# Kernel optimization log

Hardware: AMD Instinct MI355X
Metric: run time of the kernel (lower is better)

The kernel has to match this reference:

```python
import jax, jax.numpy as jnp
import numpy as np
import math

B, L, D, H = 4, 2048, 1024, 16
DK = D // H


def setup_inputs() -> dict:
    key = jax.random.key(0)
    ks = jax.random.split(key, 12)
    scale = math.sqrt(6.0 / (D + D))  # xavier_uniform for square Linear
    def lin(k):
        return jax.random.uniform(k, (D, D), jnp.float32, -scale, scale)
    inp = {
        "query": jax.random.normal(ks[0], (B, L, D), jnp.float32),
        "key": jax.random.normal(ks[1], (B, L, D), jnp.float32),
        "value": jax.random.normal(ks[2], (B, L, D), jnp.float32),
        "Wq": lin(ks[3]), "bq": jnp.zeros((D,), jnp.float32),
        "Wk": lin(ks[4]), "bk": jnp.zeros((D,), jnp.float32),
        "Wv": lin(ks[5]), "bv": jnp.zeros((D,), jnp.float32),
        "Wo": lin(ks[6]), "bo": jnp.zeros((D,), jnp.float32),
        # causal mask: True means masked (hide future positions)
        "attn_mask": jnp.triu(jnp.ones((L, L), dtype=bool), k=1),
    }
    return inp


def reference(query, key, value, Wq, bq, Wk, bk, Wv, bv, Wo, bo, attn_mask):
    def proj(x, W, b):
        # torch Linear: x @ W.T + b ; then split heads -> [B, H, L, DK]
        y = jnp.einsum('bld,ed->ble', x, W) + b
        return y.reshape(B, L, H, DK).transpose(0, 2, 1, 3)

    q = proj(query, Wq, bq)
    k = proj(key, Wk, bk)
    v = proj(value, Wv, bv)

    scores = jnp.einsum('bhqd,bhkd->bhqk', q, k) / jnp.sqrt(jnp.float32(DK))
    scores = jnp.where(attn_mask[None, None, :, :], jnp.float32(-jnp.inf), scores)
    p_attn = jax.nn.softmax(scores, axis=-1)  # dropout p=0 (eval)

    ctx = jnp.einsum('bhqk,bhkd->bhqd', p_attn, v)
    ctx = ctx.transpose(0, 2, 1, 3).reshape(B, L, D)
    out = jnp.einsum('bld,ed->ble', ctx, Wo) + bo
    return out
```

## Files before the change

kernel.cpp:

```cpp
#include <hip/hip_runtime.h>
#include <hip/hip_bf16.h>
#include <stdint.h>

typedef unsigned short u16;
typedef unsigned int u32;
typedef short short8 __attribute__((ext_vector_type(8)));
typedef float f32x4 __attribute__((ext_vector_type(4)));
typedef u32 u32x4 __attribute__((ext_vector_type(4)));
typedef u32 u32x2 __attribute__((ext_vector_type(2)));

#define DEV static __device__ __forceinline__

constexpr int Bsz = 4, Lseq = 2048, Dm = 1024, Hn = 16, Dk = 64;
constexpr float LOG2E = 1.44269504088896340736f;
constexpr float QSCALE = 0.125f * LOG2E;

DEV u16 f2bf(float x) {
    u32 u = __builtin_bit_cast(u32, x);
    return (u16)((u + 0x7fffu + ((u >> 16) & 1u)) >> 16);
}

DEV u32 pk2(float a, float b) {
    __hip_bfloat162 h = __float22bfloat162_rn(float2{a, b});
    u32 r;
    __builtin_memcpy(&r, &h, 4);
    return r;
}

DEV u32x4 ld8_cvt(const float* p) {
    f32x4 lo = *(const f32x4*)p;
    f32x4 hi = *(const f32x4*)(p + 4);
    u32x4 r;
    r[0] = pk2(lo[0], lo[1]);
    r[1] = pk2(lo[2], lo[3]);
    r[2] = pk2(hi[0], hi[1]);
    r[3] = pk2(hi[2], hi[3]);
    return r;
}

DEV void glds16(const void* g, void* l) {
    __builtin_amdgcn_global_load_lds(
        (const __attribute__((address_space(1))) void*)g,
        (__attribute__((address_space(3))) void*)l, 16, 0, 0);
}

__global__ __launch_bounds__(256) void cvt_f2b(
    const float* __restrict__ s, u16* __restrict__ d, int n8)
{
    int i = blockIdx.x * 256 + threadIdx.x;
    if (i >= n8) return;
    ((u32x4*)d)[i] = ld8_cvt(s + (long)i * 8);
}

template <int MODE>
__global__ __launch_bounds__(256) void gemm_glds(
    const u16* __restrict__ A, const u16* __restrict__ Bw,
    const float* __restrict__ bias, void* __restrict__ Cout, float scale)
{
    __shared__ u16 At[2][128 * 32];
    __shared__ u16 Bt[2][128 * 32];

    const int tid = threadIdx.x;
    const int lane = tid & 63, wid = tid >> 6;
    const int wr = wid >> 1, wc = wid & 1;
    const int mbase = blockIdx.x * 128, nbase = blockIdx.y * 128;

    f32x4 acc[4][4];
#pragma unroll
    for (int i = 0; i < 4; i++)
#pragma unroll
        for (int j = 0; j < 4; j++) acc[i][j] = (f32x4)0.f;

    const int srow = lane >> 2;
    const int sseg = (lane & 3) * 8;

    auto stage = [&](int kt, int buf) {
#pragma unroll
        for (int c = 0; c < 2; c++) {
            const int sec = wid * 2 + c;
            const long ko = (long)kt * 32 + sseg;
            glds16(A + (long)(mbase + sec * 16 + srow) * Dm + ko, &At[buf][sec * 512]);
            glds16(Bw + (long)(nbase + sec * 16 + srow) * Dm + ko, &Bt[buf][sec * 512]);
        }
    };

    stage(0, 0);
    __syncthreads();

    for (int kt = 0; kt < 32; kt++) {
        const int cur = kt & 1;
        if (kt + 1 < 32) stage(kt + 1, cur ^ 1);
        short8 af[4], bfr[4];
#pragma unroll
        for (int mf = 0; mf < 4; mf++)
            af[mf] = *(const short8*)&At[cur][(wr * 64 + mf * 16 + (lane & 15)) * 32 + (lane >> 4) * 8];
#pragma unroll
        for (int nf = 0; nf < 4; nf++)
            bfr[nf] = *(const short8*)&Bt[cur][(wc * 64 + nf * 16 + (lane & 15)) * 32 + (lane >> 4) * 8];
        __builtin_amdgcn_s_setprio(1);
#pragma unroll
        for (int mf = 0; mf < 4; mf++)
#pragma unroll
            for (int nf = 0; nf < 4; nf++)
                acc[mf][nf] = __builtin_amdgcn_mfma_f32_16x16x32_bf16(af[mf], bfr[nf], acc[mf][nf], 0, 0, 0);
        __builtin_amdgcn_s_setprio(0);
        __syncthreads();
    }

#pragma unroll
    for (int nf = 0; nf < 4; nf++) {
        const int n = nbase + wc * 64 + nf * 16 + (lane & 15);
        const float bv = bias[n];
#pragma unroll
        for (int mf = 0; mf < 4; mf++) {
            const int m0 = mbase + wr * 64 + mf * 16 + (lane >> 4) * 4;
#pragma unroll
            for (int r = 0; r < 4; r++) {
                const int m = m0 + r;
                const float v = (acc[mf][nf][r] + bv) * scale;
                if (MODE == 0) {
                    int b = m >> 11, l = m & 2047, h = n >> 6, dk = n & 63;
                    long addr = ((long)(b * Hn + h) * Lseq + l) * Dk + dk;
                    ((u16*)Cout)[addr] = f2bf(v);
                } else {
                    ((float*)Cout)[(long)m * Dm + n] = v;
                }
            }
        }
    }
}

template <int MODE, int A32>
__global__ __launch_bounds__(256) void gemm_bt(
    const void* __restrict__ Xv, const float* __restrict__ W,
    const float* __restrict__ bias, void* __restrict__ Cout, int Kdim,
    float scale)
{
    __shared__ u16 At[2][128 * 32];
    __shared__ u16 Bt[2][128 * 32];

    const int tid = threadIdx.x;
    const int lane = tid & 63, wid = tid >> 6;
    const int wr = wid >> 1, wc = wid & 1;
    const int mbase = blockIdx.x * 128, nbase = blockIdx.y * 128;

    f32x4 acc[4][4];
#pragma unroll
    for (int i = 0; i < 4; i++)
#pragma unroll
        for (int j = 0; j < 4; j++) acc[i][j] = (f32x4)0.f;

    const int NT = Kdim >> 5;

    u32x4 va[2], vb[2];
#pragma unroll
    for (int i = 0; i < 2; i++) {
        int idx = i * 256 + tid;
        int row = idx >> 2, seg = idx & 3;
        if (A32)
            va[i] = ld8_cvt((const float*)Xv + (long)(mbase + row) * Kdim + seg * 8);
        else
            va[i] = *(const u32x4*)((const u16*)Xv + (long)(mbase + row) * Kdim + seg * 8);
        vb[i] = ld8_cvt(W + (long)(nbase + row) * Kdim + seg * 8);
    }
#pragma unroll
    for (int i = 0; i < 2; i++) {
        int idx = i * 256 + tid;
        *(u32x4*)&At[0][idx * 8] = va[i];
        *(u32x4*)&Bt[0][idx * 8] = vb[i];
    }
    __syncthreads();

    for (int kt = 0; kt < NT; kt++) {
        const int cur = kt & 1;
        const bool more = (kt + 1 < NT);
        if (more) {
#pragma unroll
            for (int i = 0; i < 2; i++) {
                int idx = i * 256 + tid;
                int row = idx >> 2, seg = idx & 3;
                long ko = (long)(kt + 1) * 32 + seg * 8;
                if (A32)
                    va[i] = ld8_cvt((const float*)Xv + (long)(mbase + row) * Kdim + ko);
                else
                    va[i] = *(const u32x4*)((const u16*)Xv + (long)(mbase + row) * Kdim + ko);
                vb[i] = ld8_cvt(W + (long)(nbase + row) * Kdim + ko);
            }
        }
        short8 af[4], bfr[4];
#pragma unroll
        for (int mf = 0; mf < 4; mf++)
            af[mf] = *(const short8*)&At[cur][(wr * 64 + mf * 16 + (lane & 15)) * 32 + (lane >> 4) * 8];
#pragma unroll
        for (int nf = 0; nf < 4; nf++)
            bfr[nf] = *(const short8*)&Bt[cur][(wc * 64 + nf * 16 + (lane & 15)) * 32 + (lane >> 4) * 8];
#pragma unroll
        for (int mf = 0; mf < 4; mf++)
#pragma unroll
            for (int nf = 0; nf < 4; nf++)
                acc[mf][nf] = __builtin_amdgcn_mfma_f32_16x16x32_bf16(af[mf], bfr[nf], acc[mf][nf], 0, 0, 0);
        if (more) {
#pragma unroll
            for (int i = 0; i < 2; i++) {
                int idx = i * 256 + tid;
                *(u32x4*)&At[cur ^ 1][idx * 8] = va[i];
                *(u32x4*)&Bt[cur ^ 1][idx * 8] = vb[i];
            }
        }
        __syncthreads();
    }

#pragma unroll
    for (int nf = 0; nf < 4; nf++) {
        const int n = nbase + wc * 64 + nf * 16 + (lane & 15);
        const float bv = bias[n];
#pragma unroll
        for (int mf = 0; mf < 4; mf++) {
            const int m0 = mbase + wr * 64 + mf * 16 + (lane >> 4) * 4;
#pragma unroll
            for (int r = 0; r < 4; r++) {
                const int m = m0 + r;
                const float v = (acc[mf][nf][r] + bv) * scale;
                if (MODE == 0) {
                    int b = m >> 11, l = m & 2047, h = n >> 6, dk = n & 63;
                    long addr = ((long)(b * Hn + h) * Lseq + l) * Dk + dk;
                    ((u16*)Cout)[addr] = f2bf(v);
                } else {
                    ((float*)Cout)[(long)m * Dm + n] = v;
                }
            }
        }
    }
}

__global__ __launch_bounds__(256) void attn_fwd(
    const u16* __restrict__ Qb, const u16* __restrict__ Kb,
    const u16* __restrict__ Vb, u16* __restrict__ Ctx)
{
    __shared__ u16 Kt[2][64 * 64];
    __shared__ u16 Vt[2][64 * 64];
    __shared__ u16 Pq[4][32 * 64];

    const int tid = threadIdx.x, lane = tid & 63, w = tid >> 6;
    const int qt = gridDim.y - 1 - blockIdx.y;
    const int bh = blockIdx.x;
    const long base = (long)bh * Lseq * Dk;
    const int qw = qt * 128 + w * 32;

    const int krow_in_w = lane >> 3;
    const int kseg = lane & 7;
    const int skv = tid >> 3, sdb = (tid & 7) * 8;

    short8 qfr[2][2];
#pragma unroll
    for (int qf = 0; qf < 2; qf++)
#pragma unroll
        for (int ks = 0; ks < 2; ks++) {
            int q = qw + qf * 16 + (lane & 15);
            int d0 = ks * 32 + (lane >> 4) * 8;
            qfr[qf][ks] = *(const short8*)(Qb + base + (long)q * Dk + d0);
        }

    f32x4 accT[4][2];
#pragma unroll
    for (int i = 0; i < 4; i++)
#pragma unroll
        for (int j = 0; j < 2; j++) accT[i][j] = (f32x4)0.f;
    float m_run[2] = {-__builtin_inff(), -__builtin_inff()};
    float l_part[2] = {0.f, 0.f};

    auto stage_k = [&](int kvbase, int buf) {
#pragma unroll
        for (int c = 0; c < 2; c++) {
            int kv = w * 16 + c * 8 + krow_in_w;
            int d0 = ((kseg ^ (kv & 7)) * 8);
            glds16(Kb + base + (long)(kvbase + kv) * Dk + d0,
                   &Kt[buf][(w * 16 + c * 8) * 64]);
        }
    };

    u32x4 vr[2];
    stage_k(0, 0);
#pragma unroll
    for (int i = 0; i < 2; i++)
        vr[i] = *(const u32x4*)(Vb + base + (long)(i * 32 + skv) * Dk + sdb);
#pragma unroll
    for (int i = 0; i < 2; i++) {
        int kv = i * 32 + skv;
        const u16* pv = (const u16*)&vr[i];
#pragma unroll
        for (int j = 0; j < 8; j++) {
            int d = sdb + j;
            Vt[0][d * 64 + (kv ^ ((((d & 7) ^ (d >> 3)) & 7) << 3))] = pv[j];
        }
    }
    __syncthreads();

    const int nkv = qt * 2 + 2;
    const int myn = ((qw + 31) >> 6) + 1;

    for (int kvt = 0; kvt < nkv; kvt++) {
        const int cur = kvt & 1;
        const bool more = (kvt + 1 < nkv);
        const int kvbase = kvt * 64;

        if (more) {
            stage_k(kvbase + 64, cur ^ 1);
#pragma unroll
            for (int i = 0; i < 2; i++)
                vr[i] = *(const u32x4*)(Vb + base + (long)(kvbase + 64 + i * 32 + skv) * Dk + sdb);
        }

        if (kvt < myn) {
            f32x4 st[4][2];
#pragma unroll
            for (int i = 0; i < 4; i++)
#pragma unroll
                for (int j = 0; j < 2; j++) st[i][j] = (f32x4)0.f;
            __builtin_amdgcn_s_setprio(1);
#pragma unroll
            for (int ks = 0; ks < 2; ks++) {
                short8 kf[4];
#pragma unroll
                for (int kvf = 0; kvf < 4; kvf++) {
                    int row = kvf * 16 + (lane & 15);
                    int d0 = ks * 32 + (lane >> 4) * 8;
                    kf[kvf] = *(const short8*)&Kt[cur][row * 64 + (d0 ^ ((row & 7) << 3))];
                }
#pragma unroll
                for (int kvf = 0; kvf < 4; kvf++)
#pragma unroll
                    for (int qf = 0; qf < 2; qf++)
                        st[kvf][qf] = __builtin_amdgcn_mfma_f32_16x16x32_bf16(kf[kvf], qfr[qf][ks], st[kvf][qf], 0, 0, 0);
            }
            __builtin_amdgcn_s_setprio(0);

            if ((kvbase + 63) > qw) {
#pragma unroll
                for (int qf = 0; qf < 2; qf++) {
                    const int q = qw + qf * 16 + (lane & 15);
#pragma unroll
                    for (int kvf = 0; kvf < 4; kvf++)
#pragma unroll
                        for (int r = 0; r < 4; r++) {
                            int kv = kvbase + kvf * 16 + (lane >> 4) * 4 + r;
                            if (kv > q) st[kvf][qf][r] = -1e30f;
                        }
                }
            }

#pragma unroll
            for (int qf = 0; qf < 2; qf++) {
                float tmax = st[0][qf][0];
#pragma unroll
                for (int kvf = 0; kvf < 4; kvf++)
#pragma unroll
                    for (int r = 0; r < 4; r++) tmax = fmaxf(tmax, st[kvf][qf][r]);
                tmax = fmaxf(tmax, __shfl_xor(tmax, 16, 64));
                tmax = fmaxf(tmax, __shfl_xor(tmax, 32, 64));
                const bool norescale = __all((int)(tmax <= m_run[qf] + 8.f));
                if (!norescale) {
                    const float mnew = fmaxf(m_run[qf], tmax);
                    const float sc = __builtin_exp2f(m_run[qf] - mnew);
                    m_run[qf] = mnew;
                    l_part[qf] *= sc;
#pragma unroll
                    for (int dkf = 0; dkf < 4; dkf++)
#pragma unroll
                        for (int r = 0; r < 4; r++) accT[dkf][qf][r] *= sc;
                }
                const float mq = m_run[qf];
                float ts = 0.f;
#pragma unroll
                for (int kvf = 0; kvf < 4; kvf++)
#pragma unroll
                    for (int r = 0; r < 4; r++) {
                        float p = __builtin_exp2f(st[kvf][qf][r] - mq);
                        st[kvf][qf][r] = p;
                        ts += p;
                    }
                l_part[qf] += ts;
                const int qrow = qf * 16 + (lane & 15);
#pragma unroll
                for (int kvf = 0; kvf < 4; kvf++) {
                    u32x2 pk;
                    pk[0] = pk2(st[kvf][qf][0], st[kvf][qf][1]);
                    pk[1] = pk2(st[kvf][qf][2], st[kvf][qf][3]);
                    int kvi = (kvf * 16 + (lane >> 4) * 4) ^ ((lane & 7) << 3);
                    *(u32x2*)&Pq[w][qrow * 64 + kvi] = pk;
                }
            }

#pragma unroll
            for (int kf2 = 0; kf2 < 2; kf2++) {
                short8 vfr[4];
#pragma unroll
                for (int dkf = 0; dkf < 4; dkf++) {
                    int d = dkf * 16 + (lane & 15);
                    int kvi = (kf2 * 32 + (lane >> 4) * 8) ^ ((((d & 7) ^ (d >> 3)) & 7) << 3);
                    vfr[dkf] = *(const short8*)&Vt[cur][d * 64 + kvi];
                }
                short8 pfr[2];
#pragma unroll
                for (int qf = 0; qf < 2; qf++) {
                    int qrow = qf * 16 + (lane & 15);
                    int kvi = (kf2 * 32 + (lane >> 4) * 8) ^ ((lane & 7) << 3);
                    pfr[qf] = *(const short8*)&Pq[w][qrow * 64 + kvi];
                }
                __builtin_amdgcn_s_setprio(1);
#pragma unroll
                for (int dkf = 0; dkf < 4; dkf++)
#pragma unroll
                    for (int qf = 0; qf < 2; qf++)
                        accT[dkf][qf] = __builtin_amdgcn_mfma_f32_16x16x32_bf16(vfr[dkf], pfr[qf], accT[dkf][qf], 0, 0, 0);
                __builtin_amdgcn_s_setprio(0);
            }
        }

        if (more) {
#pragma unroll
            for (int i = 0; i < 2; i++) {
                int kv = i * 32 + skv;
                const u16* pv = (const u16*)&vr[i];
#pragma unroll
                for (int j = 0; j < 8; j++) {
                    int d = sdb + j;
                    Vt[cur ^ 1][d * 64 + (kv ^ ((((d & 7) ^ (d >> 3)) & 7) << 3))] = pv[j];
                }
            }
        }
        __syncthreads();
    }

    const int b = bh >> 4, h = bh & 15;
#pragma unroll
    for (int qf = 0; qf < 2; qf++) {
        float l = l_part[qf];
        l += __shfl_xor(l, 16, 64);
        l += __shfl_xor(l, 32, 64);
        const float inv = 1.f / l;
        const int q = qw + qf * 16 + (lane & 15);
#pragma unroll
        for (int dkf = 0; dkf < 4; dkf++) {
            const int dk0 = dkf * 16 + (lane >> 4) * 4;
            u32x2 o;
            o[0] = pk2(accT[dkf][qf][0] * inv, accT[dkf][qf][1] * inv);
            o[1] = pk2(accT[dkf][qf][2] * inv, accT[dkf][qf][3] * inv);
            long addr = ((long)b * Lseq + q) * Dm + h * Dk + dk0;
            *(u32x2*)(Ctx + addr) = o;
        }
    }
}

extern "C" void kernel_launch(void* const* d_in, const int* in_sizes, int n_in,
                              void* d_out, int out_size, void* d_ws, size_t ws_size,
                              hipStream_t stream)
{
    const float* query = (const float*)d_in[0];
    const float* key_  = (const float*)d_in[1];
    const float* value = (const float*)d_in[2];
    const float* Wq = (const float*)d_in[3];
    const float* bq = (const float*)d_in[4];
    const float* Wk = (const float*)d_in[5];
    const float* bk = (const float*)d_in[6];
    const float* Wv = (const float*)d_in[7];
    const float* bv = (const float*)d_in[8];
    const float* Wo = (const float*)d_in[9];
    const float* bo = (const float*)d_in[10];

    float* out = (float*)d_out;
    const size_t tens = (size_t)Bsz * Lseq * Dm;
    const size_t wTot = (size_t)Dm * Dm;
    u16* Qb = (u16*)d_ws;
    u16* Kb = Qb + tens;
    u16* Vb = Kb + tens;

    dim3 g(64, 8), blk(256);
    const size_t need = (4 * tens + 4 * wTot) * sizeof(u16);

    if (ws_size >= need) {
        u16* Xb = Vb + tens;
        u16* Cx = Xb;
        u16* Wqb = Xb + tens;
        u16* Wkb = Wqb + wTot;
        u16* Wvb = Wkb + wTot;
        u16* Wob = Wvb + wTot;
        const int n8w = (int)(wTot / 8), n8x = (int)(tens / 8);
        const int gw = (n8w + 255) / 256, gx = (n8x + 255) / 256;
        cvt_f2b<<<gw, blk, 0, stream>>>(Wq, Wqb, n8w);
        cvt_f2b<<<gw, blk, 0, stream>>>(Wk, Wkb, n8w);
        cvt_f2b<<<gw, blk, 0, stream>>>(Wv, Wvb, n8w);
        cvt_f2b<<<gw, blk, 0, stream>>>(Wo, Wob, n8w);

        cvt_f2b<<<gx, blk, 0, stream>>>(query, Xb, n8x);
        gemm_glds<0><<<g, blk, 0, stream>>>(Xb, Wqb, bq, Qb, QSCALE);
        cvt_f2b<<<gx, blk, 0, stream>>>(key_, Xb, n8x);
        gemm_glds<0><<<g, blk, 0, stream>>>(Xb, Wkb, bk, Kb, 1.0f);
        cvt_f2b<<<gx, blk, 0, stream>>>(value, Xb, n8x);
        gemm_glds<0><<<g, blk, 0, stream>>>(Xb, Wvb, bv, Vb, 1.0f);

        attn_fwd<<<dim3(Bsz * Hn, Lseq / 128), blk, 0, stream>>>(Qb, Kb, Vb, Cx);
        gemm_glds<1><<<g, blk, 0, stream>>>(Cx, Wob, bo, out, 1.0f);
    } else {
        u16* Cx = Vb + tens;
        gemm_bt<0, 1><<<g, blk, 0, stream>>>(query, Wq, bq, Qb, Dm, QSCALE);
        gemm_bt<0, 1><<<g, blk, 0, stream>>>(key_,  Wk, bk, Kb, Dm, 1.0f);
        gemm_bt<0, 1><<<g, blk, 0, stream>>>(value, Wv, bv, Vb, Dm, 1.0f);
        attn_fwd<<<dim3(Bsz * Hn, Lseq / 128), blk, 0, stream>>>(Qb, Kb, Vb, Cx);
        gemm_bt<1, 0><<<g, blk, 0, stream>>>(Cx, Wo, bo, out, Dm, 1.0f);
    }
}
```

Baseline: 251.8 us.

## Fuse input fp32-to-bf16 conversion into projection GEMMs and reuse workspace buffers

Adds a hybrid GEMM that reads the fp32 activations directly and converts them in registers, while the pre-converted bf16 weights are staged into LDS with direct global-to-LDS loads. This removes the three full-tensor conversion kernels and their extra write and read of the bf16 activation buffer. Workspace is repacked so the converted weights alias buffers that are dead at that point (the Wo conversion is deferred until after attention and written into the Q buffer), dropping the large-workspace branch. It also raises wave priority around the MFMA block with s_setprio. The risk is the extra fp32 global traffic on the A side inside the GEMM mainloop.

```diff
diff --git a/kernel.cpp b/kernel.cpp
--- a/kernel.cpp
+++ b/kernel.cpp
@@ -130,11 +130,9 @@
     }
 }
 
-template <int MODE, int A32>
-__global__ __launch_bounds__(256) void gemm_bt(
-    const void* __restrict__ Xv, const float* __restrict__ W,
-    const float* __restrict__ bias, void* __restrict__ Cout, int Kdim,
-    float scale)
+__global__ __launch_bounds__(256) void gemm_hyb(
+    const float* __restrict__ X, const u16* __restrict__ Bw,
+    const float* __restrict__ bias, u16* __restrict__ Cout, float scale)
 {
     __shared__ u16 At[2][128 * 32];
     __shared__ u16 Bt[2][128 * 32];
@@ -150,42 +148,45 @@
 #pragma unroll
         for (int j = 0; j < 4; j++) acc[i][j] = (f32x4)0.f;
 
-    const int NT = Kdim >> 5;
-
-    u32x4 va[2], vb[2];
-#pragma unroll
-    for (int i = 0; i < 2; i++) {
-        int idx = i * 256 + tid;
-        int row = idx >> 2, seg = idx & 3;
-        if (A32)
-            va[i] = ld8_cvt((const float*)Xv + (long)(mbase + row) * Kdim + seg * 8);
-        else
-            va[i] = *(const u32x4*)((const u16*)Xv + (long)(mbase + row) * Kdim + seg * 8);
-        vb[i] = ld8_cvt(W + (long)(nbase + row) * Kdim + seg * 8);
-    }
-#pragma unroll
-    for (int i = 0; i < 2; i++) {
-        int idx = i * 256 + tid;
-        *(u32x4*)&At[0][idx * 8] = va[i];
-        *(u32x4*)&Bt[0][idx * 8] = vb[i];
-    }
+    const int srow = lane >> 2;
+    const int sseg = (lane & 3) * 8;
+    auto stageB = [&](int kt, int buf) {
+#pragma unroll
+        for (int c = 0; c < 2; c++) {
+            const int sec = wid * 2 + c;
+            glds16(Bw + (long)(nbase + sec * 16 + srow) * Dm + (long)kt * 32 + sseg,
+                   &Bt[buf][sec * 512]);
+        }
+    };
+
+    u32x4 va[2];
+    auto loadA = [&](int kt) {
+#pragma unroll
+        for (int i = 0; i < 2; i++) {
+            int idx = i * 256 + tid;
+            int row = idx >> 2, seg = idx & 3;
+            va[i] = ld8_cvt(X + (long)(mbase + row) * Dm + (long)kt * 32 + seg * 8);
+        }
+    };
+    auto writeA = [&](int buf) {
+#pragma unroll
+        for (int i = 0; i < 2; i++) {
+            int idx = i * 256 + tid;
+            *(u32x4*)&At[buf][idx * 8] = va[i];
+        }
+    };
+
+    stageB(0, 0);
+    loadA(0);
+    writeA(0);
     __syncthreads();
 
-    for (int kt = 0; kt < NT; kt++) {
+    for (int kt = 0; kt < 32; kt++) {
         const int cur = kt & 1;
-        const bool more = (kt + 1 < NT);
+        const bool more = (kt + 1 < 32);
         if (more) {
-#pragma unroll
-            for (int i = 0; i < 2; i++) {
-                int idx = i * 256 + tid;
-                int row = idx >> 2, seg = idx & 3;
-                long ko = (long)(kt + 1) * 32 + seg * 8;
-                if (A32)
-                    va[i] = ld8_cvt((const float*)Xv + (long)(mbase + row) * Kdim + ko);
-                else
-                    va[i] = *(const u32x4*)((const u16*)Xv + (long)(mbase + row) * Kdim + ko);
-                vb[i] = ld8_cvt(W + (long)(nbase + row) * Kdim + ko);
-            }
+            stageB(kt + 1, cur ^ 1);
+            loadA(kt + 1);
         }
         short8 af[4], bfr[4];
 #pragma unroll
@@ -194,19 +195,14 @@
 #pragma unroll
         for (int nf = 0; nf < 4; nf++)
             bfr[nf] = *(const short8*)&Bt[cur][(wc * 64 + nf * 16 + (lane & 15)) * 32 + (lane >> 4) * 8];
+        __builtin_amdgcn_s_setprio(1);
 #pragma unroll
         for (int mf = 0; mf < 4; mf++)
 #pragma unroll
             for (int nf = 0; nf < 4; nf++)
                 acc[mf][nf] = __builtin_amdgcn_mfma_f32_16x16x32_bf16(af[mf], bfr[nf], acc[mf][nf], 0, 0, 0);
-        if (more) {
-#pragma unroll
-            for (int i = 0; i < 2; i++) {
-                int idx = i * 256 + tid;
-                *(u32x4*)&At[cur ^ 1][idx * 8] = va[i];
-                *(u32x4*)&Bt[cur ^ 1][idx * 8] = vb[i];
-            }
-        }
+        __builtin_amdgcn_s_setprio(0);
+        if (more) writeA(cur ^ 1);
         __syncthreads();
     }
 
@@ -221,13 +217,9 @@
             for (int r = 0; r < 4; r++) {
                 const int m = m0 + r;
                 const float v = (acc[mf][nf][r] + bv) * scale;
-                if (MODE == 0) {
-                    int b = m >> 11, l = m & 2047, h = n >> 6, dk = n & 63;
-                    long addr = ((long)(b * Hn + h) * Lseq + l) * Dk + dk;
-                    ((u16*)Cout)[addr] = f2bf(v);
-                } else {
-                    ((float*)Cout)[(long)m * Dm + n] = v;
-                }
+                int b = m >> 11, l = m & 2047, h = n >> 6, dk = n & 63;
+                long addr = ((long)(b * Hn + h) * Lseq + l) * Dk + dk;
+                Cout[addr] = f2bf(v);
             }
         }
     }
@@ -251,24 +243,6 @@
     const int kseg = lane & 7;
     const int skv = tid >> 3, sdb = (tid & 7) * 8;
 
-    short8 qfr[2][2];
-#pragma unroll
-    for (int qf = 0; qf < 2; qf++)
-#pragma unroll
-        for (int ks = 0; ks < 2; ks++) {
-            int q = qw + qf * 16 + (lane & 15);
-            int d0 = ks * 32 + (lane >> 4) * 8;
-            qfr[qf][ks] = *(const short8*)(Qb + base + (long)q * Dk + d0);
-        }
-
-    f32x4 accT[4][2];
-#pragma unroll
-    for (int i = 0; i < 4; i++)
-#pragma unroll
-        for (int j = 0; j < 2; j++) accT[i][j] = (f32x4)0.f;
-    float m_run[2] = {-__builtin_inff(), -__builtin_inff()};
-    float l_part[2] = {0.f, 0.f};
-
     auto stage_k = [&](int kvbase, int buf) {
 #pragma unroll
         for (int c = 0; c < 2; c++) {
@@ -278,6 +252,24 @@
                    &Kt[buf][(w * 16 + c * 8) * 64]);
         }
     };
+
+    short8 qfr[2][2];
+#pragma unroll
+    for (int qf = 0; qf < 2; qf++)
+#pragma unroll
+        for (int ks = 0; ks < 2; ks++) {
+            int q = qw + qf * 16 + (lane & 15);
+            int d0 = ks * 32 + (lane >> 4) * 8;
+            qfr[qf][ks] = *(const short8*)(Qb + base + (long)q * Dk + d0);
+        }
+
+    f32x4 accT[4][2];
+#pragma unroll
+    for (int i = 0; i < 4; i++)
+#pragma unroll
+        for (int j = 0; j < 2; j++) accT[i][j] = (f32x4)0.f;
+    float m_run[2] = {-__builtin_inff(), -__builtin_inff()};
+    float l_part[2] = {0.f, 0.f};
 
     u32x4 vr[2];
     stage_k(0, 0);
@@ -474,39 +466,23 @@
     u16* Qb = (u16*)d_ws;
     u16* Kb = Qb + tens;
     u16* Vb = Kb + tens;
-
-    dim3 g(64, 8), blk(256);
-    const size_t need = (4 * tens + 4 * wTot) * sizeof(u16);
-
-    if (ws_size >= need) {
-        u16* Xb = Vb + tens;
-        u16* Cx = Xb;
-        u16* Wqb = Xb + tens;
-        u16* Wkb = Wqb + wTot;
-        u16* Wvb = Wkb + wTot;
-        u16* Wob = Wvb + wTot;
-        const int n8w = (int)(wTot / 8), n8x = (int)(tens / 8);
-        const int gw = (n8w + 255) / 256, gx = (n8x + 255) / 256;
-        cvt_f2b<<<gw, blk, 0, stream>>>(Wq, Wqb, n8w);
-        cvt_f2b<<<gw, blk, 0, stream>>>(Wk, Wkb, n8w);
-        cvt_f2b<<<gw, blk, 0, stream>>>(Wv, Wvb, n8w);
-        cvt_f2b<<<gw, blk, 0, stream>>>(Wo, Wob, n8w);
-
-        cvt_f2b<<<gx, blk, 0, stream>>>(query, Xb, n8x);
-        gemm_glds<0><<<g, blk, 0, stream>>>(Xb, Wqb, bq, Qb, QSCALE);
-        cvt_f2b<<<gx, blk, 0, stream>>>(key_, Xb, n8x);
-        gemm_glds<0><<<g, blk, 0, stream>>>(Xb, Wkb, bk, Kb, 1.0f);
-        cvt_f2b<<<gx, blk, 0, stream>>>(value, Xb, n8x);
-        gemm_glds<0><<<g, blk, 0, stream>>>(Xb, Wvb, bv, Vb, 1.0f);
-
-        attn_fwd<<<dim3(Bsz * Hn, Lseq / 128), blk, 0, stream>>>(Qb, Kb, Vb, Cx);
-        gemm_glds<1><<<g, blk, 0, stream>>>(Cx, Wob, bo, out, 1.0f);
-    } else {
-        u16* Cx = Vb + tens;
-        gemm_bt<0, 1><<<g, blk, 0, stream>>>(query, Wq, bq, Qb, Dm, QSCALE);
-        gemm_bt<0, 1><<<g, blk, 0, stream>>>(key_,  Wk, bk, Kb, Dm, 1.0f);
-        gemm_bt<0, 1><<<g, blk, 0, stream>>>(value, Wv, bv, Vb, Dm, 1.0f);
-        attn_fwd<<<dim3(Bsz * Hn, Lseq / 128), blk, 0, stream>>>(Qb, Kb, Vb, Cx);
-        gemm_bt<1, 0><<<g, blk, 0, stream>>>(Cx, Wo, bo, out, Dm, 1.0f);
-    }
-}
+    u16* Cx = Vb + tens;
+    u16* Wqb = Cx;
+    u16* Wkb = Wqb + wTot;
+    u16* Wvb = Wkb + wTot;
+    u16* Wob = Qb;
+
+    dim3 blk(256), g(64, 8);
+    const int n8w = (int)(wTot / 8);
+    const int gw = (n8w + 255) / 256;
+
+    cvt_f2b<<<gw, blk, 0, stream>>>(Wq, Wqb, n8w);
+    cvt_f2b<<<gw, blk, 0, stream>>>(Wk, Wkb, n8w);
+    cvt_f2b<<<gw, blk, 0, stream>>>(Wv, Wvb, n8w);
+    gemm_hyb<<<g, blk, 0, stream>>>(query, Wqb, bq, Qb, QSCALE);
+    gemm_hyb<<<g, blk, 0, stream>>>(key_,  Wkb, bk, Kb, 1.0f);
+    gemm_hyb<<<g, blk, 0, stream>>>(value, Wvb, bv, Vb, 1.0f);
+    attn_fwd<<<dim3(Bsz * Hn, Lseq / 128), blk, 0, stream>>>(Qb, Kb, Vb, Cx);
+    cvt_f2b<<<gw, blk, 0, stream>>>(Wo, Wob, n8w);
+    gemm_glds<1><<<g, blk, 0, stream>>>(Cx, Wob, bo, out, 1.0f);
+}
```

New measurement: 243.6 us. -3.2%, faster.
